# Performance work log

Measured on AMD Instinct MI355X. Metric: run time of the kernel, lower is better.

The kernel has to match this reference:

```python
import jax, jax.numpy as jnp
import numpy as np
from jax import lax

B, C_IN, H, W = 16, 64, 64, 64
C_OUT, K, P, NC = 128, 3, 1, 512
PS = C_IN * K * K  # 576 patch feature size


def setup_inputs() -> dict:
    key = jax.random.key(0)
    k0, k1, k2, k3 = jax.random.split(key, 4)
    x = jax.random.normal(k0, (B, C_IN, H, W), jnp.float32)
    cluster_centers = jax.random.normal(k1, (NC, PS), jnp.float32)
    temp = jnp.ones((1,), jnp.float32)
    weight = jax.random.normal(k2, (C_OUT, C_IN, K, K), jnp.float32) * 0.05
    bias = jax.random.normal(k3, (C_OUT,), jnp.float32) * 0.05
    return {"x": x, "cluster_centers": cluster_centers, "temp": temp,
            "weight": weight, "bias": bias}


def _forward(x, cluster_centers, temp, weight, bias):
    Bx, C, Hx, Wx = x.shape
    t = temp.reshape(())  # scalar temperature
    # F.unfold: patches ordered (c, kh, kw) along feature dim -> [B, C*K*K, H, W]
    patches = lax.conv_general_dilated_patches(
        x, (K, K), (1, 1), padding=((P, P), (P, P)))
    L = Hx * Wx  # number of blocks; equals Wx*Wx (H==W, same-padding, stride 1)
    cols = patches.reshape(Bx, PS, L)               # this_patch
    flat = cols.transpose(0, 2, 1).reshape(-1, PS)  # [N, PS] flat_patches
    # torch.cdist (p=2): stable squared-distance expansion, single GEMM
    d2 = (jnp.sum(flat * flat, axis=1, keepdims=True)
          + jnp.sum(cluster_centers * cluster_centers, axis=1)[None, :]
          - 2.0 * (flat @ cluster_centers.T))
    dist = jnp.sqrt(jnp.maximum(d2, 0.0))           # [N, NC]
    soft = jax.nn.softmax(-dist * t, axis=1)        # soft assignments
    transformed = soft @ cluster_centers            # [N, PS]
    final = (t * transformed + flat) / (t + 1.0)
    # Faithful to the original's view_as: raw reshape WITHOUT transposing back
    final = final.reshape(Bx, PS, L)
    # F.fold(output_size=(W*K, W*K), kernel=K, padding=P, stride=K):
    # non-overlapping tiles on padded canvas, then crop P from each side.
    # (b, c, kh, kw, bh, bw) -> (b, c, bh, kh, bw, kw)
    tile = (final.reshape(Bx, C, K, K, Wx, Wx)
                 .transpose(0, 1, 4, 2, 5, 3)
                 .reshape(Bx, C, Wx * K, Wx * K))
    # crop offset P=1 at the top/left; bottom/right of cropped region is zero
    x_refold = jnp.pad(tile[:, :, P:, P:], ((0, 0), (0, 0), (0, P), (0, P)))
    # F.conv2d(..., stride=kernel_size, padding=padding)
    out = lax.conv_general_dilated(
        x_refold, weight, window_strides=(K, K), padding=((P, P), (P, P)),
        dimension_numbers=("NCHW", "OIHW", "NCHW"))
    return out + bias[None, :, None, None]


def reference(x, cluster_centers, temp, weight, bias):
    return _forward(x, cluster_centers, temp, weight, bias)
```

## Files before the change

### kernel.cpp

```cpp
#include <hip/hip_runtime.h>
#include <stdint.h>

typedef __bf16 bf16;
typedef bf16 bf16x2 __attribute__((ext_vector_type(2)));
typedef bf16 bf16x8 __attribute__((ext_vector_type(8)));
typedef float f32x4 __attribute__((ext_vector_type(4)));

static constexpr int B_    = 16;
static constexpr int C_IN  = 64;
static constexpr int H_    = 64;
static constexpr int W_    = 64;
static constexpr int C_OUT = 128;
static constexpr int NC    = 512;
static constexpr int PS    = 576;
static constexpr int L_    = H_ * W_;
static constexpr int NR    = B_ * L_;

#define DEVI __device__ __forceinline__

DEVI void gload_lds16(const void* g, void* l) {
  __builtin_amdgcn_global_load_lds(
      (const __attribute__((address_space(1))) uint32_t*)g,
      (__attribute__((address_space(3))) uint32_t*)l, 16, 0, 0);
}


__global__ void prep_w_kernel(const float* __restrict__ w, bf16* __restrict__ WB,
                              bf16* __restrict__ ccT) {
  int i = blockIdx.x * 256 + threadIdx.x;
  if (i < C_OUT * PS) WB[i] = (bf16)w[i];
  if (i < 64 * NC) ccT[(size_t)PS * NC + i] = (bf16)0.f;
}

__global__ void prep_cc_kernel(const float* __restrict__ cc, bf16* __restrict__ ccB,
                               bf16* __restrict__ ccT, float* __restrict__ cn) {
  int j = blockIdx.x;
  const float* src = cc + (size_t)j * PS;
  float s = 0.f;
  for (int p = threadIdx.x; p < PS; p += 256) {
    float v = src[p];
    bf16 bv = (bf16)v;
    ccB[(size_t)j * PS + p] = bv;
    ccT[(size_t)p * NC + j] = bv;
    float fv = (float)bv;
    s += fv * fv;
  }
  for (int o = 32; o; o >>= 1) s += __shfl_xor(s, o);
  __shared__ float red[4];
  int lane = threadIdx.x & 63, wid = threadIdx.x >> 6;
  if (lane == 0) red[wid] = s;
  __syncthreads();
  if (threadIdx.x == 0) cn[j] = red[0] + red[1] + red[2] + red[3];
}

static constexpr int XS_STRIDE = 66;
static constexpr int XS_PLANE  = 64 * XS_STRIDE;
static constexpr int XS_OFF    = 2;

__global__ void __launch_bounds__(256, 4) patch_kernel(
    const float* __restrict__ x, bf16* __restrict__ flatB,
    float* __restrict__ rn, float* __restrict__ rsum) {
  __shared__ bf16 xs[XS_OFF + 3 * XS_PLANE + 64];
  const int bh = blockIdx.x;
  const int b = bh >> 6, h = bh & 63;
  const size_t bOff = (size_t)b * (C_IN * L_);
#pragma unroll
  for (int it = 0; it < 12; ++it) {
    int idx = threadIdx.x + it * 256;
    int plane = idx >> 10;
    int rem = idx & 1023;
    int c = rem >> 4;
    int f4 = rem & 15;
    int y = h + plane - 1;
    int e = XS_OFF + plane * XS_PLANE + c * XS_STRIDE + f4 * 4;
    bf16x2 lo = {(bf16)0.f, (bf16)0.f}, hi = {(bf16)0.f, (bf16)0.f};
    if ((unsigned)y < 64u) {
      float4 v = *(const float4*)(x + bOff + (size_t)c * L_ + y * 64 + f4 * 4);
      lo = bf16x2{(bf16)v.x, (bf16)v.y};
      hi = bf16x2{(bf16)v.z, (bf16)v.w};
    }
    *(bf16x2*)(xs + e) = lo;
    *(bf16x2*)(xs + e + 2) = hi;
  }
  __syncthreads();

  const int lane = threadIdx.x & 63, wid = threadIdx.x >> 6;
  int eb[8], km[8];
#pragma unroll
  for (int q = 0; q < 8; q++) {
    int p = lane * 8 + q;
    int c = p / 9, r9 = p - c * 9;
    int kh = r9 / 3, kw = r9 - kh * 3;
    eb[q] = kh * XS_PLANE + c * XS_STRIDE + (kw - 1);
    km[q] = kw - 1;
  }
  int ebt[8], kmt[8];
  {
    int pl = (lane & 7) * 8;
#pragma unroll
    for (int q = 0; q < 8; q++) {
      int p = 512 + pl + q;
      int c = p / 9, r9 = p - c * 9;
      int kh = r9 / 3, kw = r9 - kh * 3;
      ebt[q] = kh * XS_PLANE + c * XS_STRIDE + (kw - 1);
      kmt[q] = kw - 1;
    }
  }
  for (int it = 0; it < 16; ++it) {
    int w = wid * 16 + it;
    int row = bh * 64 + w;
    bf16* outp = flatB + (size_t)row * PS;
    float s = 0.f;
    bf16x8 v;
#pragma unroll
    for (int q = 0; q < 8; q++) {
      int xx = w + km[q];
      float fv = ((unsigned)xx < 64u) ? (float)xs[XS_OFF + eb[q] + w] : 0.f;
      v[q] = (bf16)fv;
      s += fv * fv;
    }
    *(bf16x8*)(outp + lane * 8) = v;
    if (lane < 8) {
      bf16x8 v2;
#pragma unroll
      for (int q = 0; q < 8; q++) {
        int xx = w + kmt[q];
        float fv = ((unsigned)xx < 64u) ? (float)xs[XS_OFF + ebt[q] + w] : 0.f;
        v2[q] = (bf16)fv;
        s += fv * fv;
      }
      *(bf16x8*)(outp + 512 + lane * 8) = v2;
    }
    for (int o = 32; o; o >>= 1) s += __shfl_xor(s, o);
    if (lane == 0) { rn[row] = s; rsum[row] = 0.f; }
  }
}

template <int EPI, int GX>
__global__ void __launch_bounds__(512, 4) gemm_nt(
    const bf16* __restrict__ A, int lda, const bf16* __restrict__ Bm, int ldb,
    int M, int N, int Kd,
    const float* __restrict__ e0, const float* __restrict__ e1,
    const float* __restrict__ e2, const bf16* flatB,
    float* outF, bf16* outB, int ldc) {
  const int blk = blockIdx.x;
  const int xcd = blk & 7;
  const int k = blk >> 3;
  const int ypx = (gridDim.x >> 3) / GX;
  const int bx = k % GX;
  const int by = xcd * ypx + k / GX;
  const int m0 = by * 256, n0 = bx * 128;

  __shared__ bf16 As[256 * 64];
  __shared__ bf16 Bs[128 * 64];
  const int tid = threadIdx.x;
  const int lane = tid & 63;
  const int wid = tid >> 6;
  const int wr = wid >> 1;
  const int wc = wid & 1;

  const int srow = tid >> 3;
  const int sch = ((tid & 7) ^ (srow & 7)) * 8;
  const bf16* gA = A + (size_t)(m0 + srow) * lda + sch;
  const bf16* gB = Bm + (size_t)(n0 + srow) * ldb + sch;

  const int lrow = lane & 15;
  const int kq = lane >> 4;
  const int axor = lrow & 7;
  const int arow = (wr * 64 + lrow) * 64;
  const int brow = (wc * 64 + lrow) * 64;

  f32x4 acc[4][4];
#pragma unroll
  for (int i = 0; i < 4; i++)
#pragma unroll
    for (int j = 0; j < 4; j++) acc[i][j] = f32x4{0.f, 0.f, 0.f, 0.f};

  const int nk = Kd >> 6;
  for (int kt = 0; kt < nk; ++kt) {
    __syncthreads();
    const bf16* ga = gA + kt * 64;
    const bf16* gb = gB + kt * 64;
#pragma unroll
    for (int q = 0; q < 4; ++q)
      gload_lds16(ga + (size_t)(q * 64) * lda, As + q * 4096 + tid * 8);
#pragma unroll
    for (int q = 0; q < 2; ++q)
      gload_lds16(gb + (size_t)(q * 64) * ldb, Bs + q * 4096 + tid * 8);
    __syncthreads();
#pragma unroll
    for (int h = 0; h < 2; ++h) {
      const int cs = ((h * 4 + kq) ^ axor) * 8;
      bf16x8 af[4], bfr[4];
#pragma unroll
      for (int i = 0; i < 4; i++) af[i] = *(const bf16x8*)(As + arow + i * 1024 + cs);
#pragma unroll
      for (int j = 0; j < 4; j++) bfr[j] = *(const bf16x8*)(Bs + brow + j * 1024 + cs);
#pragma unroll
      for (int i = 0; i < 4; i++)
#pragma unroll
        for (int j = 0; j < 4; j++)
          acc[i][j] = __builtin_amdgcn_mfma_f32_16x16x32_bf16(af[i], bfr[j], acc[i][j], 0, 0, 0);
    }
  }

  const int rb = m0 + wr * 64 + kq * 4;
  const int cb = n0 + wc * 64 + lrow;
  if constexpr (EPI == 1) {
    float t = e2[0];
#pragma unroll
    for (int i = 0; i < 4; i++) {
      float rowsum[4] = {0.f, 0.f, 0.f, 0.f};
#pragma unroll
      for (int j = 0; j < 4; j++) {
        int col = cb + j * 16;
        float cnv = e1[col];
#pragma unroll
        for (int r = 0; r < 4; r++) {
          int row = rb + i * 16 + r;
          float d2 = e0[row] + cnv - 2.f * acc[i][j][r];
          float e = __expf(-t * sqrtf(fmaxf(d2, 0.f)));
          outB[(size_t)row * ldc + col] = (bf16)e;
          rowsum[r] += e;
        }
      }
#pragma unroll
      for (int r = 0; r < 4; r++) {
        float s = rowsum[r];
        s += __shfl_xor(s, 1);
        s += __shfl_xor(s, 2);
        s += __shfl_xor(s, 4);
        s += __shfl_xor(s, 8);
        if (lrow == 0) atomicAdd(outF + rb + i * 16 + r, s);
      }
    }
  } else {
    float t = e0[0];
    float inv = 1.f / (t + 1.f);
#pragma unroll
    for (int i = 0; i < 4; i++) {
      float arw[4];
#pragma unroll
      for (int r = 0; r < 4; r++) arw[r] = t * inv / e1[rb + i * 16 + r];
#pragma unroll
      for (int j = 0; j < 4; j++) {
        int col = cb + j * 16;
        if (col < N) {
#pragma unroll
          for (int r = 0; r < 4; r++) {
            int row = rb + i * 16 + r;
            float fl = (float)flatB[(size_t)row * PS + col];
            float v = acc[i][j][r] * arw[r] + fl * inv;
            outB[(size_t)row * ldc + col] = (bf16)v;
          }
        }
      }
    }
  }
}

__global__ void __launch_bounds__(256, 4) gemm3_kernel(
    const bf16* __restrict__ A, const bf16* __restrict__ F,
    const float* __restrict__ bias, float* __restrict__ outF) {
  const size_t bz = blockIdx.z;
  const bf16* Fb = F + bz * (size_t)L_ * PS;
  float* outp = outF + bz * (size_t)C_OUT * L_;
  const int n0 = blockIdx.x * 128;

  __shared__ bf16 As[128 * 64];
  __shared__ bf16 Bs[128 * 64];
  const int tid = threadIdx.x;
  const int lane = tid & 63;
  const int wid = tid >> 6;
  const int wr = wid >> 1, wc = wid & 1;

  const int srow = tid >> 3;
  const int sch = ((tid & 7) ^ (srow & 7)) * 8;
  const bf16* gA = A + (size_t)srow * PS + sch;
  bf16* lA = As + tid * 8;

  const int lrow = lane & 15;
  const int kq = lane >> 4;
  const int axor = lrow & 7;
  const int arow = (wr * 64 + lrow) * 64;
  const int brow = (wc * 64 + lrow) * 64;

  f32x4 acc[4][4];
#pragma unroll
  for (int i = 0; i < 4; i++)
#pragma unroll
    for (int j = 0; j < 4; j++) acc[i][j] = f32x4{0.f, 0.f, 0.f, 0.f};

  const int nk = PS / 64;
  for (int kt = 0; kt < nk; ++kt) {
    __syncthreads();
    const bf16* ga = gA + kt * 64;
#pragma unroll
    for (int q = 0; q < 4; ++q)
      gload_lds16(ga + (size_t)(q * 32) * PS, lA + q * 2048);
#pragma unroll
    for (int ps = 0; ps < 2; ++ps) {
      int id = tid + ps * 256;
      int pp = id >> 4;
      int lc = id & 15;
      int pl = 2 * pp;
      int pg = kt * 64 + pl;
      const bf16* s0 = Fb + (size_t)pg * L_ + n0 + lc * 8;
      bf16x8 v0 = *(const bf16x8*)s0;
      bf16x8 v1 = *(const bf16x8*)(s0 + L_);
      int l8 = n0 + lc * 8;
      int oh = l8 >> 6;
      bool ow0 = (l8 & 63) == 0;
      int r90 = pg % 9;
      int kh0 = r90 / 3, kw0 = r90 - 3 * kh0;
      int r91 = (pg + 1) % 9;
      int kh1 = r91 / 3, kw1 = r91 - 3 * kh1;
      if (oh == 0 && kh0 == 0) {
#pragma unroll
        for (int e = 0; e < 8; e++) v0[e] = (bf16)0.f;
      }
      if (ow0 && kw0 == 0) v0[0] = (bf16)0.f;
      if (oh == 0 && kh1 == 0) {
#pragma unroll
        for (int e = 0; e < 8; e++) v1[e] = (bf16)0.f;
      }
      if (ow0 && kw1 == 0) v1[0] = (bf16)0.f;
#pragma unroll
      for (int e = 0; e < 8; ++e) {
        int l = lc * 8 + e;
        int addr = l * 64 + (((pl >> 3) ^ (l & 7)) << 3) + (pl & 7);
        *(bf16x2*)(Bs + addr) = bf16x2{v0[e], v1[e]};
      }
    }
    __syncthreads();
#pragma unroll
    for (int h = 0; h < 2; ++h) {
      const int cs = ((h * 4 + kq) ^ axor) * 8;
      bf16x8 af[4], bfr[4];
#pragma unroll
      for (int i = 0; i < 4; i++) af[i] = *(const bf16x8*)(As + arow + i * 1024 + cs);
#pragma unroll
      for (int j = 0; j < 4; j++) bfr[j] = *(const bf16x8*)(Bs + brow + j * 1024 + cs);
#pragma unroll
      for (int i = 0; i < 4; i++)
#pragma unroll
        for (int j = 0; j < 4; j++)
          acc[i][j] = __builtin_amdgcn_mfma_f32_16x16x32_bf16(af[i], bfr[j], acc[i][j], 0, 0, 0);
    }
  }

  const int rb = wr * 64 + kq * 4;
  const int cb = n0 + wc * 64 + lrow;
#pragma unroll
  for (int i = 0; i < 4; i++) {
#pragma unroll
    for (int j = 0; j < 4; j++) {
      int col = cb + j * 16;
#pragma unroll
      for (int r = 0; r < 4; r++) {
        int row = rb + i * 16 + r;
        outp[(size_t)row * L_ + col] = acc[i][j][r] + bias[row];
      }
    }
  }
}


extern "C" void kernel_launch(void* const* d_in, const int* in_sizes, int n_in,
                              void* d_out, int out_size, void* d_ws, size_t ws_size,
                              hipStream_t stream) {
  (void)in_sizes; (void)n_in; (void)out_size; (void)ws_size;
  const float* x    = (const float*)d_in[0];
  const float* cc   = (const float*)d_in[1];
  const float* tp   = (const float*)d_in[2];
  const float* w    = (const float*)d_in[3];
  const float* bias = (const float*)d_in[4];
  float* out = (float*)d_out;

  char* ws = (char*)d_ws;
  size_t off = 0;
  auto alloc = [&](size_t bytes) {
    char* p = ws + off;
    off += (bytes + 255) & ~(size_t)255;
    return p;
  };
  bf16* ccB   = (bf16*)alloc((size_t)NC * PS * 2);
  bf16* ccT   = (bf16*)alloc((size_t)640 * NC * 2);
  float* cn   = (float*)alloc((size_t)NC * 4);
  bf16* WB    = (bf16*)alloc((size_t)C_OUT * PS * 2);
  float* rn   = (float*)alloc((size_t)NR * 4);
  float* rsum = (float*)alloc((size_t)NR * 4);
  bf16* flatB = (bf16*)alloc((size_t)NR * PS * 2);
  bf16* E     = (bf16*)alloc((size_t)NR * NC * 2);

  prep_w_kernel<<<dim3(288), dim3(256), 0, stream>>>(w, WB, ccT);
  prep_cc_kernel<<<dim3(NC), dim3(256), 0, stream>>>(cc, ccB, ccT, cn);
  patch_kernel<<<dim3(B_ * H_), dim3(256), 0, stream>>>(x, flatB, rn, rsum);
  gemm_nt<1, 4><<<dim3((NR / 256) * (NC / 128)), dim3(512), 0, stream>>>(
      flatB, PS, ccB, PS, NR, NC, PS, rn, cn, tp, nullptr, rsum, E, NC);
  gemm_nt<2, 5><<<dim3((NR / 256) * 5), dim3(512), 0, stream>>>(
      E, NC, ccT, NC, NR, PS, NC, tp, rsum, nullptr, flatB, nullptr, flatB, PS);
  gemm3_kernel<<<dim3(L_ / 128, 1, B_), dim3(256), 0, stream>>>(WB, flatB, bias, out);
}
```

Before: 241.2 us.

## Fuse distance GEMM, softmax and centroid GEMM into one kernel keeping E in LDS

Replaces the two separate GEMM launches with a single kernel per 64-row tile. It computes all 512 cluster distances, stores the exponentials in LDS, reduces the row sums in shared memory, then does the second GEMM against the transposed centers straight from LDS. This removes the global E matrix round trip, the rsum buffer and its atomics. In exchange it uses a large LDS union, fewer rows per block, launch bounds of 2, and a second GEMM that reloads centroid tiles many times per block with a narrow 64-column output per pass.

```diff
diff --git a/kernel.cpp b/kernel.cpp
--- a/kernel.cpp
+++ b/kernel.cpp
@@ -15,6 +15,7 @@
 static constexpr int PS    = 576;
 static constexpr int L_    = H_ * W_;
 static constexpr int NR    = B_ * L_;
+static constexpr int EPAD  = 514;
 
 #define DEVI __device__ __forceinline__
 
@@ -59,7 +60,7 @@
 
 __global__ void __launch_bounds__(256, 4) patch_kernel(
     const float* __restrict__ x, bf16* __restrict__ flatB,
-    float* __restrict__ rn, float* __restrict__ rsum) {
+    float* __restrict__ rn) {
   __shared__ bf16 xs[XS_OFF + 3 * XS_PLANE + 64];
   const int bh = blockIdx.x;
   const int b = bh >> 6, h = bh & 63;
@@ -132,95 +133,91 @@
       *(bf16x8*)(outp + 512 + lane * 8) = v2;
     }
     for (int o = 32; o; o >>= 1) s += __shfl_xor(s, o);
-    if (lane == 0) { rn[row] = s; rsum[row] = 0.f; }
-  }
-}
-
-template <int EPI, int GX>
-__global__ void __launch_bounds__(512, 4) gemm_nt(
-    const bf16* __restrict__ A, int lda, const bf16* __restrict__ Bm, int ldb,
-    int M, int N, int Kd,
-    const float* __restrict__ e0, const float* __restrict__ e1,
-    const float* __restrict__ e2, const bf16* flatB,
-    float* outF, bf16* outB, int ldc) {
-  const int blk = blockIdx.x;
-  const int xcd = blk & 7;
-  const int k = blk >> 3;
-  const int ypx = (gridDim.x >> 3) / GX;
-  const int bx = k % GX;
-  const int by = xcd * ypx + k / GX;
-  const int m0 = by * 256, n0 = bx * 128;
-
-  __shared__ bf16 As[256 * 64];
-  __shared__ bf16 Bs[128 * 64];
+    if (lane == 0) rn[row] = s;
+  }
+}
+
+__global__ void __launch_bounds__(256, 2) gemm12_kernel(
+    const bf16* __restrict__ flat, const bf16* __restrict__ ccB,
+    const bf16* __restrict__ ccT, const float* __restrict__ rn,
+    const float* __restrict__ cn, const float* __restrict__ tp,
+    bf16* finalB) {
+  __shared__ union {
+    struct { bf16 As[64 * 64]; bf16 Bs[512 * 64]; } a;
+    struct { bf16 E[64 * EPAD]; bf16 Bs2[64 * 64]; } b;
+  } u;
+  __shared__ float parts[4 * 64];
+
   const int tid = threadIdx.x;
   const int lane = tid & 63;
-  const int wid = tid >> 6;
-  const int wr = wid >> 1;
-  const int wc = wid & 1;
-
-  const int srow = tid >> 3;
-  const int sch = ((tid & 7) ^ (srow & 7)) * 8;
-  const bf16* gA = A + (size_t)(m0 + srow) * lda + sch;
-  const bf16* gB = Bm + (size_t)(n0 + srow) * ldb + sch;
-
+  const int wc = tid >> 6;
   const int lrow = lane & 15;
   const int kq = lane >> 4;
   const int axor = lrow & 7;
-  const int arow = (wr * 64 + lrow) * 64;
-  const int brow = (wc * 64 + lrow) * 64;
-
-  f32x4 acc[4][4];
+  const int m0 = blockIdx.x * 64;
+
+  const int srow = tid >> 3;
+  const int slot = tid & 7;
+  const int sch = ((slot ^ (srow & 7)) * 8);
+
+  const float t = tp[0];
+
+  f32x4 acc[4][8];
 #pragma unroll
   for (int i = 0; i < 4; i++)
 #pragma unroll
-    for (int j = 0; j < 4; j++) acc[i][j] = f32x4{0.f, 0.f, 0.f, 0.f};
-
-  const int nk = Kd >> 6;
-  for (int kt = 0; kt < nk; ++kt) {
+    for (int j = 0; j < 8; j++) acc[i][j] = f32x4{0.f, 0.f, 0.f, 0.f};
+
+  const bf16* gA = flat + (size_t)(m0 + srow) * PS + sch;
+  const bf16* gB = ccB + (size_t)srow * PS + sch;
+
+  for (int kt = 0; kt < 9; ++kt) {
     __syncthreads();
     const bf16* ga = gA + kt * 64;
     const bf16* gb = gB + kt * 64;
-#pragma unroll
-    for (int q = 0; q < 4; ++q)
-      gload_lds16(ga + (size_t)(q * 64) * lda, As + q * 4096 + tid * 8);
-#pragma unroll
-    for (int q = 0; q < 2; ++q)
-      gload_lds16(gb + (size_t)(q * 64) * ldb, Bs + q * 4096 + tid * 8);
+    gload_lds16(ga, u.a.As + tid * 8);
+    gload_lds16(ga + (size_t)32 * PS, u.a.As + 2048 + tid * 8);
+#pragma unroll
+    for (int q = 0; q < 16; ++q)
+      gload_lds16(gb + (size_t)(q * 32) * PS, u.a.Bs + q * 2048 + tid * 8);
     __syncthreads();
 #pragma unroll
     for (int h = 0; h < 2; ++h) {
       const int cs = ((h * 4 + kq) ^ axor) * 8;
-      bf16x8 af[4], bfr[4];
-#pragma unroll
-      for (int i = 0; i < 4; i++) af[i] = *(const bf16x8*)(As + arow + i * 1024 + cs);
-#pragma unroll
-      for (int j = 0; j < 4; j++) bfr[j] = *(const bf16x8*)(Bs + brow + j * 1024 + cs);
+      bf16x8 af[4], bfr[8];
 #pragma unroll
       for (int i = 0; i < 4; i++)
-#pragma unroll
-        for (int j = 0; j < 4; j++)
+        af[i] = *(const bf16x8*)(u.a.As + (i * 16 + lrow) * 64 + cs);
+#pragma unroll
+      for (int j = 0; j < 8; j++)
+        bfr[j] = *(const bf16x8*)(u.a.Bs + (wc * 128 + j * 16 + lrow) * 64 + cs);
+#pragma unroll
+      for (int i = 0; i < 4; i++)
+#pragma unroll
+        for (int j = 0; j < 8; j++)
           acc[i][j] = __builtin_amdgcn_mfma_f32_16x16x32_bf16(af[i], bfr[j], acc[i][j], 0, 0, 0);
     }
   }
 
-  const int rb = m0 + wr * 64 + kq * 4;
-  const int cb = n0 + wc * 64 + lrow;
-  if constexpr (EPI == 1) {
-    float t = e2[0];
+  __syncthreads();
+  {
+    float cnv[8];
+#pragma unroll
+    for (int j = 0; j < 8; j++) cnv[j] = cn[wc * 128 + j * 16 + lrow];
 #pragma unroll
     for (int i = 0; i < 4; i++) {
       float rowsum[4] = {0.f, 0.f, 0.f, 0.f};
-#pragma unroll
-      for (int j = 0; j < 4; j++) {
-        int col = cb + j * 16;
-        float cnv = e1[col];
+      float rnv[4];
+#pragma unroll
+      for (int r = 0; r < 4; r++) rnv[r] = rn[m0 + i * 16 + kq * 4 + r];
+#pragma unroll
+      for (int j = 0; j < 8; j++) {
 #pragma unroll
         for (int r = 0; r < 4; r++) {
-          int row = rb + i * 16 + r;
-          float d2 = e0[row] + cnv - 2.f * acc[i][j][r];
+          float d2 = rnv[r] + cnv[j] - 2.f * acc[i][j][r];
           float e = __expf(-t * sqrtf(fmaxf(d2, 0.f)));
-          outB[(size_t)row * ldc + col] = (bf16)e;
+          int row_l = i * 16 + kq * 4 + r;
+          u.b.E[row_l * EPAD + wc * 128 + j * 16 + lrow] = (bf16)e;
           rowsum[r] += e;
         }
       }
@@ -231,29 +228,48 @@
         s += __shfl_xor(s, 2);
         s += __shfl_xor(s, 4);
         s += __shfl_xor(s, 8);
-        if (lrow == 0) atomicAdd(outF + rb + i * 16 + r, s);
-      }
-    }
-  } else {
-    float t = e0[0];
-    float inv = 1.f / (t + 1.f);
+        if (lrow == 0) parts[wc * 64 + i * 16 + kq * 4 + r] = s;
+      }
+    }
+  }
+
+  const float inv = 1.f / (t + 1.f);
+  for (int pt = 0; pt < 9; ++pt) {
+    const int p0 = pt * 64;
+    f32x4 acc2[4];
+#pragma unroll
+    for (int i = 0; i < 4; i++) acc2[i] = f32x4{0.f, 0.f, 0.f, 0.f};
+    for (int ks = 0; ks < 8; ++ks) {
+      __syncthreads();
+      const bf16* gb = ccT + (size_t)(p0 + srow) * NC + ks * 64 + sch;
+      gload_lds16(gb, u.b.Bs2 + tid * 8);
+      gload_lds16(gb + (size_t)32 * NC, u.b.Bs2 + 2048 + tid * 8);
+      __syncthreads();
+#pragma unroll
+      for (int h = 0; h < 2; ++h) {
+        const int ck = ks * 8 + h * 4 + kq;
+        const int cs = ((h * 4 + kq) ^ axor) * 8;
+        bf16x8 af2[4];
+#pragma unroll
+        for (int i = 0; i < 4; i++)
+          af2[i] = *(const bf16x8*)(u.b.E + (i * 16 + lrow) * EPAD + ck * 8);
+        bf16x8 b2 = *(const bf16x8*)(u.b.Bs2 + (wc * 16 + lrow) * 64 + cs);
+#pragma unroll
+        for (int i = 0; i < 4; i++)
+          acc2[i] = __builtin_amdgcn_mfma_f32_16x16x32_bf16(af2[i], b2, acc2[i], 0, 0, 0);
+      }
+    }
+    const int col = p0 + wc * 16 + lrow;
 #pragma unroll
     for (int i = 0; i < 4; i++) {
-      float arw[4];
-#pragma unroll
-      for (int r = 0; r < 4; r++) arw[r] = t * inv / e1[rb + i * 16 + r];
-#pragma unroll
-      for (int j = 0; j < 4; j++) {
-        int col = cb + j * 16;
-        if (col < N) {
-#pragma unroll
-          for (int r = 0; r < 4; r++) {
-            int row = rb + i * 16 + r;
-            float fl = (float)flatB[(size_t)row * PS + col];
-            float v = acc[i][j][r] * arw[r] + fl * inv;
-            outB[(size_t)row * ldc + col] = (bf16)v;
-          }
-        }
+#pragma unroll
+      for (int r = 0; r < 4; r++) {
+        int row_l = i * 16 + kq * 4 + r;
+        float rs = parts[row_l] + parts[64 + row_l] + parts[128 + row_l] + parts[192 + row_l];
+        size_t idx = (size_t)(m0 + row_l) * PS + col;
+        float fl = (float)finalB[idx];
+        float v = acc2[i][r] * (t * inv / rs) + fl * inv;
+        finalB[idx] = (bf16)v;
       }
     }
   }
@@ -389,16 +405,12 @@
   float* cn   = (float*)alloc((size_t)NC * 4);
   bf16* WB    = (bf16*)alloc((size_t)C_OUT * PS * 2);
   float* rn   = (float*)alloc((size_t)NR * 4);
-  float* rsum = (float*)alloc((size_t)NR * 4);
   bf16* flatB = (bf16*)alloc((size_t)NR * PS * 2);
-  bf16* E     = (bf16*)alloc((size_t)NR * NC * 2);
 
   prep_w_kernel<<<dim3(288), dim3(256), 0, stream>>>(w, WB, ccT);
   prep_cc_kernel<<<dim3(NC), dim3(256), 0, stream>>>(cc, ccB, ccT, cn);
-  patch_kernel<<<dim3(B_ * H_), dim3(256), 0, stream>>>(x, flatB, rn, rsum);
-  gemm_nt<1, 4><<<dim3((NR / 256) * (NC / 128)), dim3(512), 0, stream>>>(
-      flatB, PS, ccB, PS, NR, NC, PS, rn, cn, tp, nullptr, rsum, E, NC);
-  gemm_nt<2, 5><<<dim3((NR / 256) * 5), dim3(512), 0, stream>>>(
-      E, NC, ccT, NC, NR, PS, NC, tp, rsum, nullptr, flatB, nullptr, flatB, PS);
+  patch_kernel<<<dim3(B_ * H_), dim3(256), 0, stream>>>(x, flatB, rn);
+  gemm12_kernel<<<dim3(NR / 64), dim3(256), 0, stream>>>(
+      flatB, ccB, ccT, rn, cn, tp, flatB);
   gemm3_kernel<<<dim3(L_ / 128, 1, B_), dim3(256), 0, stream>>>(WB, flatB, bias, out);
 }
```

New measurement: 481.0 us. 99.4% more time.
